# Kernel tuning notes

Hardware: AMD Instinct MI355X
Metric: run time of the kernel (lower is better)

Reference implementation:

```python
import jax, jax.numpy as jnp
import numpy as np

B, L, W = 4096, 30, 5          # batch, MAX_TOKEN_LENGTH, WINDOW_SIZE
A, E = 30, 128                 # ALPHABET_SIZE, embedding dim
C = 40                         # OUT_CHANNELS
H, T = 128, 3                  # LSTM_UNITS, num CRF tags
LIN = W * C                    # 200
EPS = 1e-5


def setup_inputs():
    key = jax.random.key(0)
    ks = jax.random.split(key, 24)
    def rn(k, shape, s=0.1):
        return jax.random.normal(k, shape, jnp.float32) * s
    return {
        'x': jax.random.randint(ks[0], (B, L, W), 0, A, jnp.int32),
        'emb': rn(ks[1], (A, E), 1.0),
        'conv_w': rn(ks[2], (C, E, 3)),
        'conv_b': rn(ks[3], (C,)),
        'bn1_g': 1.0 + rn(ks[4], (C,)),
        'bn1_b': rn(ks[5], (C,)),
        'bn1_m': rn(ks[6], (C,)),
        'bn1_v': 0.5 + jax.random.uniform(ks[7], (C,), jnp.float32),
        'w_ih_f': rn(ks[8], (4 * H, LIN)),
        'w_hh_f': rn(ks[9], (4 * H, H)),
        'b_f': rn(ks[10], (4 * H,)),
        'w_ih_b': rn(ks[11], (4 * H, LIN)),
        'w_hh_b': rn(ks[12], (4 * H, H)),
        'b_b': rn(ks[13], (4 * H,)),
        'bn2_g': 1.0 + rn(ks[14], (2 * H,)),
        'bn2_b': rn(ks[15], (2 * H,)),
        'bn2_m': rn(ks[16], (2 * H,)),
        'bn2_v': 0.5 + jax.random.uniform(ks[17], (2 * H,), jnp.float32),
        'fc_w': rn(ks[18], (T, 2 * H)),
        'fc_b': rn(ks[19], (T,)),
        'trans': rn(ks[20], (T, T)),
        'start_t': rn(ks[21], (T,)),
        'end_t': rn(ks[22], (T,)),
    }


def _lstm_dir(seq, w_ih, w_hh, b, reverse):
    # seq: [B, L, F]; torch gate order i, f, g, o
    xs = jnp.einsum('blf,gf->lbg', seq, w_ih) + b  # [L, B, 4H]
    h0 = jnp.zeros((seq.shape[0], H), seq.dtype)
    def step(carry, xt):
        h, c = carry
        z = xt + h @ w_hh.T
        i, f, g, o = jnp.split(z, 4, axis=-1)
        c = jax.nn.sigmoid(f) * c + jax.nn.sigmoid(i) * jnp.tanh(g)
        h = jax.nn.sigmoid(o) * jnp.tanh(c)
        return (h, c), h
    _, hs = jax.lax.scan(step, (h0, h0), xs, reverse=reverse)
    return hs.transpose(1, 0, 2)  # [B, L, H]


def _viterbi(emis, mask, trans, start_t, end_t):
    # emis: [B, L, T], mask: [B, L] bool
    score = start_t + emis[:, 0]                      # [B, T]
    def step(score, inp):
        e_t, m_t = inp                                # [B, T], [B]
        cand = score[:, :, None] + trans              # [B, Tprev, Tnext]
        ptr = jnp.argmax(cand, axis=1)                # [B, T]
        new = jnp.max(cand, axis=1) + e_t
        return jnp.where(m_t[:, None], new, score), ptr
    score, hist = jax.lax.scan(
        step, score, (emis[:, 1:].transpose(1, 0, 2), mask[:, 1:].T))
    score = score + end_t
    best = jnp.max(score, axis=1)                     # [B] path scores
    last = jnp.argmax(score, axis=1)                  # [B]
    def back(tag, inp):
        h_t, m_t = inp
        prev = jnp.take_along_axis(h_t, tag[:, None], axis=1)[:, 0]
        tag = jnp.where(m_t, prev, tag)
        return tag, tag
    _, ys = jax.lax.scan(back, last, (hist, mask[:, 1:].T), reverse=True)
    tags = jnp.concatenate([ys, last[None]], axis=0).T  # [B, L]
    return best, tags


def reference(x, emb, conv_w, conv_b, bn1_g, bn1_b, bn1_m, bn1_v,
              w_ih_f, w_hh_f, b_f, w_ih_b, w_hh_b, b_b,
              bn2_g, bn2_b, bn2_m, bn2_v, fc_w, fc_b, trans, start_t, end_t):
    mask = x[:, :, 2] > 0                             # [B, L]
    e = emb[x.reshape(B * L, W)]                      # [N, W, E]  (dropout=eval noop)
    e = e.transpose(0, 2, 1)                          # [N, E, W]
    y = jax.lax.conv_general_dilated(
        e, conv_w, (1,), [(1, 1)],
        dimension_numbers=('NCH', 'OIH', 'NCH')) + conv_b[:, None]
    # BatchNorm1d (inference, running stats)
    y = (y - bn1_m[:, None]) * (bn1_g / jnp.sqrt(bn1_v + EPS))[:, None] + bn1_b[:, None]
    y = jax.nn.relu(y)
    # MaxPool1d(k=3, stride=1, pad=1): length preserved
    y = jax.lax.reduce_window(y, -jnp.inf, jax.lax.max,
                              (1, 1, 3), (1, 1, 1),
                              [(0, 0), (0, 0), (1, 1)])
    y = y.reshape(B, L, LIN)                          # torch.flatten is channel-major = row-major reshape
    hf = _lstm_dir(y, w_ih_f, w_hh_f, b_f, False)
    hb = _lstm_dir(y, w_ih_b, w_hh_b, b_b, True)
    h = jnp.concatenate([hf, hb], axis=-1)            # [B, L, 2H]
    h = (h - bn2_m) * (bn2_g / jnp.sqrt(bn2_v + EPS)) + bn2_b
    emis = h @ fc_w.T + fc_b                          # [B, L, T]
    return _viterbi(emis, mask, trans, start_t, end_t)
```

## Files before the change

kernel.cpp:

```cpp
#include <hip/hip_runtime.h>
#include <math.h>

#define BB    4096
#define LL    30
#define WW    5
#define CC    40
#define HH    128
#define TT    3
#define KA    328
#define KPAD  352
#define NB    32
#define ASTR  360
#define ZSTR  520
#define CW    1056

#define WS_P    0
#define WS_BC   3600
#define WS_BG   3648
#define WS_WFC  4672
#define WS_EB   5440
#define WS_WBF  5504
#define WS_EMIS (5504 + 540672)

typedef __bf16 bf16x8 __attribute__((ext_vector_type(8)));
typedef float  f32x4  __attribute__((ext_vector_type(4)));
typedef unsigned short u16x8 __attribute__((ext_vector_type(8)));

__device__ __forceinline__ float sigm(float x) {
    return __builtin_amdgcn_rcpf(1.0f + __expf(-x));
}
__device__ __forceinline__ float tanh_fast(float x) {
    return 2.0f * __builtin_amdgcn_rcpf(1.0f + __expf(-2.0f * x)) - 1.0f;
}
__device__ __forceinline__ unsigned short f2bf(float f) {
    unsigned u = __builtin_bit_cast(unsigned, f);
    return (unsigned short)((u + 0x7FFFu + ((u >> 16) & 1u)) >> 16);
}
__device__ __forceinline__ float bf2f(unsigned short h) {
    unsigned u = ((unsigned)h) << 16;
    return __builtin_bit_cast(float, u);
}

__global__ void prep_kernel(const float* __restrict__ emb, const float* __restrict__ conv_w,
                            const float* __restrict__ conv_b,
                            const float* __restrict__ bn1_g, const float* __restrict__ bn1_b,
                            const float* __restrict__ bn1_m, const float* __restrict__ bn1_v,
                            const float* __restrict__ w_ih_f, const float* __restrict__ w_hh_f,
                            const float* __restrict__ b_f,
                            const float* __restrict__ w_ih_b, const float* __restrict__ w_hh_b,
                            const float* __restrict__ b_b,
                            const float* __restrict__ bn2_g, const float* __restrict__ bn2_b,
                            const float* __restrict__ bn2_m, const float* __restrict__ bn2_v,
                            const float* __restrict__ fc_w, const float* __restrict__ fc_b,
                            float* __restrict__ ws)
{
    const int gid = blockIdx.x * blockDim.x + threadIdx.x;
    const int gsz = gridDim.x * blockDim.x;

    for (int idx = gid; idx < 3600; idx += gsz) {
        int k = idx / 1200, rem = idx % 1200, a = rem / 40, c = rem % 40;
        float s1 = bn1_g[c] / sqrtf(bn1_v[c] + 1e-5f);
        float acc = 0.f;
        for (int e = 0; e < 128; ++e)
            acc += emb[a * 128 + e] * conv_w[(c * 128 + e) * 3 + k];
        ws[WS_P + idx] = acc * s1;
    }
    for (int c = gid; c < CC; c += gsz) {
        float s1 = bn1_g[c] / sqrtf(bn1_v[c] + 1e-5f);
        ws[WS_BC + c] = (conv_b[c] - bn1_m[c]) * s1 + bn1_b[c];
    }
    for (int i = gid; i < 1024; i += gsz) {
        int d = i >> 9, g = i & 511;
        ws[WS_BG + i] = d ? b_b[g] : b_f[g];
    }
    for (int i = gid; i < 768; i += gsz) {
        int d = i / 384, r = i % 384, t = r / 128, u = r % 128;
        int j = d * 128 + u;
        float s2 = bn2_g[j] / sqrtf(bn2_v[j] + 1e-5f);
        ws[WS_WFC + i] = fc_w[t * 256 + j] * s2;
    }
    for (int t = gid; t < TT; t += gsz) {
        float acc = fc_b[t];
        for (int j = 0; j < 256; ++j) {
            float s2 = bn2_g[j] / sqrtf(bn2_v[j] + 1e-5f);
            acc += fc_w[t * 256 + j] * (bn2_b[j] - bn2_m[j] * s2);
        }
        ws[WS_EB + t] = acc;
    }
    unsigned short* wsu = (unsigned short*)ws;
    for (int i = gid; i < 2 * 512 * CW; i += gsz) {
        int d = i / (512 * CW), r = i % (512 * CW);
        int n = r / CW, q = r % CW;
        int Ks = q / 96, t = q % 96, s = t / 32, k32 = t % 32;
        int k = Ks * 32 + k32;
        int u = n >> 2, g = n & 3, row = g * 128 + u;
        const float* wih = d ? w_ih_b : w_ih_f;
        const float* whh = d ? w_hh_b : w_hh_f;
        float w = (k < 200) ? wih[row * 200 + k]
                            : ((k < KA) ? whh[row * 128 + (k - 200)] : 0.f);
        unsigned short t0 = f2bf(w);
        float r1 = w - bf2f(t0);
        unsigned short t1 = f2bf(r1);
        unsigned short t2 = f2bf(r1 - bf2f(t1));
        wsu[2 * WS_WBF + i] = (s == 0) ? t0 : ((s == 1) ? t1 : t2);
    }
}

__global__ __launch_bounds__(512, 1)
void lstm_kernel(const int* __restrict__ x, float* __restrict__ ws)
{
    __shared__ unsigned short AhU[NB * ASTR];
    __shared__ unsigned short AlU[NB * ASTR];
    __shared__ unsigned short AmU[NB * ASTR];
    __shared__ float Zs[NB * ZSTR];
    __shared__ float Pp_s[3600];
    __shared__ float Wfc_s[384];
    __shared__ float biasC_s[40];

    const int tid = threadIdx.x;
    const int d   = blockIdx.x & 1;
    const int b0  = (blockIdx.x >> 1) * NB;

    const unsigned short* __restrict__ Wb =
        (const unsigned short*)ws + 2 * WS_WBF + d * (512 * CW);
    float* emis = ws + WS_EMIS + d * (BB * LL * TT);

    for (int i = tid; i < 3600; i += 512) Pp_s[i] = ws[WS_P + i];
    for (int i = tid; i < 384;  i += 512) Wfc_s[i] = ws[WS_WFC + d * 384 + i];
    for (int i = tid; i < 40;   i += 512) biasC_s[i] = ws[WS_BC + i];
    for (int i = tid; i < NB * ASTR / 2; i += 512) {
        ((unsigned*)AhU)[i] = 0u;
        ((unsigned*)AlU)[i] = 0u;
        ((unsigned*)AmU)[i] = 0u;
    }

    const int lane = tid & 63;
    const int wv   = tid >> 6;
    const int quad = lane >> 4;
    const int ml   = lane & 15;

    const unsigned short* __restrict__ Wn0 = Wb + (wv * 64 +  0 + ml) * CW + quad * 8;
    const unsigned short* __restrict__ Wn1 = Wb + (wv * 64 + 16 + ml) * CW + quad * 8;
    const unsigned short* __restrict__ Wn2 = Wb + (wv * 64 + 32 + ml) * CW + quad * 8;
    const unsigned short* __restrict__ Wn3 = Wb + (wv * 64 + 48 + ml) * CW + quad * 8;

    const int ug = tid & 127;
    const int rg = tid >> 7;
    const float* bgp = ws + WS_BG + d * 512;
    const float bI = bgp[ug], bF = bgp[128 + ug], bG = bgp[256 + ug], bO = bgp[384 + ug];

    float cst[8];
    #pragma unroll
    for (int i = 0; i < 8; ++i) cst[i] = 0.f;

    __syncthreads();

    for (int step = 0; step < LL; ++step) {
        const int l = d ? (LL - 1 - step) : step;

        for (int p = tid; p < NB * CC; p += 512) {
            int bb = p / CC, c = p % CC;
            const int* tok = x + (((b0 + bb) * LL) + l) * WW;
            int t0 = tok[0], t1 = tok[1], t2 = tok[2], t3 = tok[3], t4 = tok[4];
            float bc = biasC_s[c];
            float a0 = bc + Pp_s[(30 + t0) * 40 + c] + Pp_s[(60 + t1) * 40 + c];
            float a1 = bc + Pp_s[t0 * 40 + c] + Pp_s[(30 + t1) * 40 + c] + Pp_s[(60 + t2) * 40 + c];
            float a2 = bc + Pp_s[t1 * 40 + c] + Pp_s[(30 + t2) * 40 + c] + Pp_s[(60 + t3) * 40 + c];
            float a3 = bc + Pp_s[t2 * 40 + c] + Pp_s[(30 + t3) * 40 + c] + Pp_s[(60 + t4) * 40 + c];
            float a4 = bc + Pp_s[t3 * 40 + c] + Pp_s[(30 + t4) * 40 + c];
            a0 = fmaxf(a0, 0.f); a1 = fmaxf(a1, 0.f); a2 = fmaxf(a2, 0.f);
            a3 = fmaxf(a3, 0.f); a4 = fmaxf(a4, 0.f);
            float f[5];
            f[0] = fmaxf(a0, a1);
            f[1] = fmaxf(fmaxf(a0, a1), a2);
            f[2] = fmaxf(fmaxf(a1, a2), a3);
            f[3] = fmaxf(fmaxf(a2, a3), a4);
            f[4] = fmaxf(a3, a4);
            int base = bb * ASTR + c * 5;
            #pragma unroll
            for (int j = 0; j < 5; ++j) {
                unsigned short h0 = f2bf(f[j]);
                float r1 = f[j] - bf2f(h0);
                unsigned short h1 = f2bf(r1);
                unsigned short h2 = f2bf(r1 - bf2f(h1));
                AhU[base + j] = h0;
                AlU[base + j] = h1;
                AmU[base + j] = h2;
            }
        }
        __syncthreads();

        f32x4 acc[2][4];
        #pragma unroll
        for (int mt = 0; mt < 2; ++mt)
            #pragma unroll
            for (int nt = 0; nt < 4; ++nt)
                acc[mt][nt] = (f32x4){0.f, 0.f, 0.f, 0.f};

#define WLOAD(B, P, KS)                                                        \
        {                                                                      \
            B[0] = *(const bf16x8*)((P) + (KS) * 96);                          \
            B[1] = *(const bf16x8*)((P) + (KS) * 96 + 32);                     \
            B[2] = *(const bf16x8*)((P) + (KS) * 96 + 64);                     \
        }
#define GEMM6(B, NT)                                                           \
        {                                                                      \
            acc[0][NT] = __builtin_amdgcn_mfma_f32_16x16x32_bf16(a0[0], B[0], acc[0][NT], 0, 0, 0); \
            acc[0][NT] = __builtin_amdgcn_mfma_f32_16x16x32_bf16(a0[1], B[0], acc[0][NT], 0, 0, 0); \
            acc[0][NT] = __builtin_amdgcn_mfma_f32_16x16x32_bf16(a0[0], B[1], acc[0][NT], 0, 0, 0); \
            acc[0][NT] = __builtin_amdgcn_mfma_f32_16x16x32_bf16(a0[1], B[1], acc[0][NT], 0, 0, 0); \
            acc[0][NT] = __builtin_amdgcn_mfma_f32_16x16x32_bf16(a0[0], B[2], acc[0][NT], 0, 0, 0); \
            acc[0][NT] = __builtin_amdgcn_mfma_f32_16x16x32_bf16(a0[2], B[0], acc[0][NT], 0, 0, 0); \
            acc[1][NT] = __builtin_amdgcn_mfma_f32_16x16x32_bf16(a1[0], B[0], acc[1][NT], 0, 0, 0); \
            acc[1][NT] = __builtin_amdgcn_mfma_f32_16x16x32_bf16(a1[1], B[0], acc[1][NT], 0, 0, 0); \
            acc[1][NT] = __builtin_amdgcn_mfma_f32_16x16x32_bf16(a1[0], B[1], acc[1][NT], 0, 0, 0); \
            acc[1][NT] = __builtin_amdgcn_mfma_f32_16x16x32_bf16(a1[1], B[1], acc[1][NT], 0, 0, 0); \
            acc[1][NT] = __builtin_amdgcn_mfma_f32_16x16x32_bf16(a1[0], B[2], acc[1][NT], 0, 0, 0); \
            acc[1][NT] = __builtin_amdgcn_mfma_f32_16x16x32_bf16(a1[2], B[0], acc[1][NT], 0, 0, 0); \
        }

        bf16x8 bufA[3], bufB[3];
        WLOAD(bufA, Wn0, 0)

        #pragma unroll
        for (int Ks = 0; Ks < 11; ++Ks) {
            const int ko = Ks * 32 + quad * 8;
            bf16x8 a0[3], a1[3];
            a0[0] = *(const bf16x8*)&AhU[ml * ASTR + ko];
            a0[1] = *(const bf16x8*)&AlU[ml * ASTR + ko];
            a0[2] = *(const bf16x8*)&AmU[ml * ASTR + ko];
            a1[0] = *(const bf16x8*)&AhU[(16 + ml) * ASTR + ko];
            a1[1] = *(const bf16x8*)&AlU[(16 + ml) * ASTR + ko];
            a1[2] = *(const bf16x8*)&AmU[(16 + ml) * ASTR + ko];

            WLOAD(bufB, Wn1, Ks)
            GEMM6(bufA, 0)
            WLOAD(bufA, Wn2, Ks)
            GEMM6(bufB, 1)
            WLOAD(bufB, Wn3, Ks)
            GEMM6(bufA, 2)
            if (Ks < 10) WLOAD(bufA, Wn0, Ks + 1)
            GEMM6(bufB, 3)
        }
#undef WLOAD
#undef GEMM6

        #pragma unroll
        for (int mt = 0; mt < 2; ++mt)
            #pragma unroll
            for (int nt = 0; nt < 4; ++nt) {
                int col = wv * 64 + nt * 16 + ml;
                int row0 = mt * 16 + quad * 4;
                #pragma unroll
                for (int i = 0; i < 4; ++i)
                    Zs[(row0 + i) * ZSTR + col] = acc[mt][nt][i];
            }
        __syncthreads();

        #pragma unroll
        for (int i = 0; i < 8; ++i) {
            int r = rg * 8 + i;
            float4 z = *(const float4*)&Zs[r * ZSTR + ug * 4];
            float zi = z.x + bI, zf = z.y + bF, zg = z.z + bG, zo = z.w + bO;
            float cn = sigm(zf) * cst[i] + sigm(zi) * tanh_fast(zg);
            cst[i] = cn;
            float h = sigm(zo) * tanh_fast(cn);
            unsigned short h0 = f2bf(h);
            float r1 = h - bf2f(h0);
            unsigned short h1 = f2bf(r1);
            unsigned short h2 = f2bf(r1 - bf2f(h1));
            int idx = r * ASTR + 200 + ug;
            AhU[idx] = h0;
            AlU[idx] = h1;
            AmU[idx] = h2;
        }
        __syncthreads();

        if (tid < 192) {
            int bb = tid / 6, r6 = tid % 6, t = r6 >> 1, seg = r6 & 1;
            int base = bb * ASTR + 200 + seg * 64;
            const float* wfc = &Wfc_s[t * 128 + seg * 64];
            float s = 0.f;
            #pragma unroll
            for (int i = 0; i < 8; ++i) {
                u16x8 v0 = *(const u16x8*)&AhU[base + i * 8];
                u16x8 v1 = *(const u16x8*)&AlU[base + i * 8];
                u16x8 v2 = *(const u16x8*)&AmU[base + i * 8];
                #pragma unroll
                for (int j = 0; j < 8; ++j) {
                    float h = bf2f(v0[j]) + bf2f(v1[j]) + bf2f(v2[j]);
                    s += h * wfc[i * 8 + j];
                }
            }
            s += __shfl_xor(s, 1);
            if (seg == 0)
                emis[(((b0 + bb) * LL) + l) * TT + t] = s;
        }
    }
}

__global__ void viterbi_kernel(const int* __restrict__ x, const float* __restrict__ ws,
                               const float* __restrict__ trans,
                               const float* __restrict__ start_t,
                               const float* __restrict__ end_t,
                               float* __restrict__ out)
{
    int b = blockIdx.x * blockDim.x + threadIdx.x;
    if (b >= BB) return;
    const float* eF = ws + WS_EMIS;
    const float* eB = ws + WS_EMIS + BB * LL * TT;
    const float eb0 = ws[WS_EB + 0], eb1 = ws[WS_EB + 1], eb2 = ws[WS_EB + 2];
    float tr[9];
    #pragma unroll
    for (int i = 0; i < 9; ++i) tr[i] = trans[i];

    int base = b * LL * TT;
    float s0 = start_t[0] + eF[base + 0] + eB[base + 0] + eb0;
    float s1 = start_t[1] + eF[base + 1] + eB[base + 1] + eb1;
    float s2 = start_t[2] + eF[base + 2] + eB[base + 2] + eb2;

    unsigned hist[LL - 1];
    unsigned maskbits = 0;

    #pragma unroll
    for (int l = 1; l < LL; ++l) {
        bool m = x[(b * LL + l) * WW + 2] > 0;
        if (m) maskbits |= (1u << l);
        int idx = base + l * TT;
        float e0 = eF[idx + 0] + eB[idx + 0] + eb0;
        float e1 = eF[idx + 1] + eB[idx + 1] + eb1;
        float e2 = eF[idx + 2] + eB[idx + 2] + eb2;

        float ns[3]; int pt[3];
        #pragma unroll
        for (int nt = 0; nt < 3; ++nt) {
            float c0 = s0 + tr[0 * 3 + nt];
            float c1 = s1 + tr[1 * 3 + nt];
            float c2 = s2 + tr[2 * 3 + nt];
            int p = 0; float bc = c0;
            if (c1 > bc) { bc = c1; p = 1; }
            if (c2 > bc) { bc = c2; p = 2; }
            ns[nt] = bc; pt[nt] = p;
        }
        ns[0] += e0; ns[1] += e1; ns[2] += e2;
        hist[l - 1] = (unsigned)pt[0] | ((unsigned)pt[1] << 2) | ((unsigned)pt[2] << 4);
        if (m) { s0 = ns[0]; s1 = ns[1]; s2 = ns[2]; }
    }
    s0 += end_t[0]; s1 += end_t[1]; s2 += end_t[2];
    float best = s0; int last = 0;
    if (s1 > best) { best = s1; last = 1; }
    if (s2 > best) { best = s2; last = 2; }

    out[b] = best;
    float* tags = out + BB + b * LL;
    int tag = last;
    tags[LL - 1] = (float)last;
    #pragma unroll
    for (int l = LL - 1; l >= 1; --l) {
        int prev = (int)((hist[l - 1] >> (2 * tag)) & 3u);
        if (maskbits & (1u << l)) tag = prev;
        tags[l - 1] = (float)tag;
    }
}

extern "C" void kernel_launch(void* const* d_in, const int* in_sizes, int n_in,
                              void* d_out, int out_size, void* d_ws, size_t ws_size,
                              hipStream_t stream)
{
    const int*   x      = (const int*)  d_in[0];
    const float* emb    = (const float*)d_in[1];
    const float* conv_w = (const float*)d_in[2];
    const float* conv_b = (const float*)d_in[3];
    const float* bn1_g  = (const float*)d_in[4];
    const float* bn1_b  = (const float*)d_in[5];
    const float* bn1_m  = (const float*)d_in[6];
    const float* bn1_v  = (const float*)d_in[7];
    const float* w_ih_f = (const float*)d_in[8];
    const float* w_hh_f = (const float*)d_in[9];
    const float* b_f    = (const float*)d_in[10];
    const float* w_ih_b = (const float*)d_in[11];
    const float* w_hh_b = (const float*)d_in[12];
    const float* b_b    = (const float*)d_in[13];
    const float* bn2_g  = (const float*)d_in[14];
    const float* bn2_b  = (const float*)d_in[15];
    const float* bn2_m  = (const float*)d_in[16];
    const float* bn2_v  = (const float*)d_in[17];
    const float* fc_w   = (const float*)d_in[18];
    const float* fc_b   = (const float*)d_in[19];
    const float* trans  = (const float*)d_in[20];
    const float* start_t= (const float*)d_in[21];
    const float* end_t  = (const float*)d_in[22];

    float* ws  = (float*)d_ws;
    float* out = (float*)d_out;

    prep_kernel<<<256, 256, 0, stream>>>(emb, conv_w, conv_b,
                                         bn1_g, bn1_b, bn1_m, bn1_v,
                                         w_ih_f, w_hh_f, b_f,
                                         w_ih_b, w_hh_b, b_b,
                                         bn2_g, bn2_b, bn2_m, bn2_v,
                                         fc_w, fc_b, ws);
    lstm_kernel<<<256, 512, 0, stream>>>(x, ws);
    viterbi_kernel<<<16, 256, 0, stream>>>(x, ws, trans, start_t, end_t, out);
}
```

Before: 841.8 us.

## Double-buffer conv features and compute LSTM gates directly from MFMA accumulators

Splits the shared A operand into double-buffered feature tiles and a separate hidden-state tile, so the next timestep's conv features are computed while the current step's emission projection runs, before a single barrier. The MFMA operands are swapped so each lane's accumulator holds the four i,f,g,o gates of one unit, which removes the Zs shared-memory round trip and one barrier per step. The weight packing is changed so the hidden-state columns start at K offset 224. The emission output is delayed by one step and flushed after the loop, which adds some bookkeeping and extra shared memory for the second feature buffer.

```diff
diff --git a/kernel.cpp b/kernel.cpp
--- a/kernel.cpp
+++ b/kernel.cpp
@@ -8,10 +8,9 @@
 #define HH    128
 #define TT    3
 #define KA    328
-#define KPAD  352
 #define NB    32
-#define ASTR  360
-#define ZSTR  520
+#define FSTR  232
+#define HSTR  136
 #define CW    1056
 
 #define WS_P    0
@@ -97,7 +96,7 @@
         const float* wih = d ? w_ih_b : w_ih_f;
         const float* whh = d ? w_hh_b : w_hh_f;
         float w = (k < 200) ? wih[row * 200 + k]
-                            : ((k < KA) ? whh[row * 128 + (k - 200)] : 0.f);
+                            : ((k >= 224) ? whh[row * 128 + (k - 224)] : 0.f);
         unsigned short t0 = f2bf(w);
         float r1 = w - bf2f(t0);
         unsigned short t1 = f2bf(r1);
@@ -109,10 +108,8 @@
 __global__ __launch_bounds__(512, 1)
 void lstm_kernel(const int* __restrict__ x, float* __restrict__ ws)
 {
-    __shared__ unsigned short AhU[NB * ASTR];
-    __shared__ unsigned short AlU[NB * ASTR];
-    __shared__ unsigned short AmU[NB * ASTR];
-    __shared__ float Zs[NB * ZSTR];
+    __shared__ unsigned short Fh[2][NB * FSTR], Fl[2][NB * FSTR], Fm[2][NB * FSTR];
+    __shared__ unsigned short Hh[NB * HSTR], Hl[NB * HSTR], Hm[NB * HSTR];
     __shared__ float Pp_s[3600];
     __shared__ float Wfc_s[384];
     __shared__ float biasC_s[40];
@@ -128,10 +125,11 @@
     for (int i = tid; i < 3600; i += 512) Pp_s[i] = ws[WS_P + i];
     for (int i = tid; i < 384;  i += 512) Wfc_s[i] = ws[WS_WFC + d * 384 + i];
     for (int i = tid; i < 40;   i += 512) biasC_s[i] = ws[WS_BC + i];
-    for (int i = tid; i < NB * ASTR / 2; i += 512) {
-        ((unsigned*)AhU)[i] = 0u;
-        ((unsigned*)AlU)[i] = 0u;
-        ((unsigned*)AmU)[i] = 0u;
+    for (int i = tid; i < NB * FSTR; i += 512) {
+        ((unsigned*)Fh)[i] = 0u; ((unsigned*)Fl)[i] = 0u; ((unsigned*)Fm)[i] = 0u;
+    }
+    for (int i = tid; i < NB * HSTR / 2; i += 512) {
+        ((unsigned*)Hh)[i] = 0u; ((unsigned*)Hl)[i] = 0u; ((unsigned*)Hm)[i] = 0u;
     }
 
     const int lane = tid & 63;
@@ -144,51 +142,67 @@
     const unsigned short* __restrict__ Wn2 = Wb + (wv * 64 + 32 + ml) * CW + quad * 8;
     const unsigned short* __restrict__ Wn3 = Wb + (wv * 64 + 48 + ml) * CW + quad * 8;
 
-    const int ug = tid & 127;
-    const int rg = tid >> 7;
     const float* bgp = ws + WS_BG + d * 512;
-    const float bI = bgp[ug], bF = bgp[128 + ug], bG = bgp[256 + ug], bO = bgp[384 + ug];
-
-    float cst[8];
+    int   un[4];
+    float bIv[4], bFv[4], bGv[4], bOv[4];
     #pragma unroll
-    for (int i = 0; i < 8; ++i) cst[i] = 0.f;
+    for (int nt = 0; nt < 4; ++nt) {
+        int u = wv * 16 + nt * 4 + quad;
+        un[nt]  = u;
+        bIv[nt] = bgp[u];
+        bFv[nt] = bgp[128 + u];
+        bGv[nt] = bgp[256 + u];
+        bOv[nt] = bgp[384 + u];
+    }
+
+    float cst[2][4];
+    #pragma unroll
+    for (int mt = 0; mt < 2; ++mt)
+        #pragma unroll
+        for (int nt = 0; nt < 4; ++nt) cst[mt][nt] = 0.f;
 
     __syncthreads();
 
+#define DO_FEATURES(LPOS, BUF)                                                 \
+    for (int p = tid; p < NB * CC; p += 512) {                                 \
+        int bb = p / CC, c = p % CC;                                           \
+        const int* tok = x + (((b0 + bb) * LL) + (LPOS)) * WW;                 \
+        int t0 = tok[0], t1 = tok[1], t2 = tok[2], t3 = tok[3], t4 = tok[4];   \
+        float bc = biasC_s[c];                                                 \
+        float a0 = bc + Pp_s[(30 + t0) * 40 + c] + Pp_s[(60 + t1) * 40 + c];   \
+        float a1 = bc + Pp_s[t0 * 40 + c] + Pp_s[(30 + t1) * 40 + c] + Pp_s[(60 + t2) * 40 + c]; \
+        float a2 = bc + Pp_s[t1 * 40 + c] + Pp_s[(30 + t2) * 40 + c] + Pp_s[(60 + t3) * 40 + c]; \
+        float a3 = bc + Pp_s[t2 * 40 + c] + Pp_s[(30 + t3) * 40 + c] + Pp_s[(60 + t4) * 40 + c]; \
+        float a4 = bc + Pp_s[t3 * 40 + c] + Pp_s[(30 + t4) * 40 + c];          \
+        a0 = fmaxf(a0, 0.f); a1 = fmaxf(a1, 0.f); a2 = fmaxf(a2, 0.f);         \
+        a3 = fmaxf(a3, 0.f); a4 = fmaxf(a4, 0.f);                              \
+        float f[5];                                                            \
+        f[0] = fmaxf(a0, a1);                                                  \
+        f[1] = fmaxf(fmaxf(a0, a1), a2);                                       \
+        f[2] = fmaxf(fmaxf(a1, a2), a3);                                       \
+        f[3] = fmaxf(fmaxf(a2, a3), a4);                                       \
+        f[4] = fmaxf(a3, a4);                                                  \
+        int base = bb * FSTR + c * 5;                                          \
+        _Pragma("unroll")                                                      \
+        for (int j = 0; j < 5; ++j) {                                          \
+            unsigned short h0 = f2bf(f[j]);                                    \
+            float r1 = f[j] - bf2f(h0);                                        \
+            unsigned short h1 = f2bf(r1);                                      \
+            unsigned short h2 = f2bf(r1 - bf2f(h1));                           \
+            Fh[BUF][base + j] = h0;                                            \
+            Fl[BUF][base + j] = h1;                                            \
+            Fm[BUF][base + j] = h2;                                            \
+        }                                                                      \
+    }
+
+    {
+        const int l0 = d ? (LL - 1) : 0;
+        DO_FEATURES(l0, 0)
+    }
+    __syncthreads();
+
     for (int step = 0; step < LL; ++step) {
-        const int l = d ? (LL - 1 - step) : step;
-
-        for (int p = tid; p < NB * CC; p += 512) {
-            int bb = p / CC, c = p % CC;
-            const int* tok = x + (((b0 + bb) * LL) + l) * WW;
-            int t0 = tok[0], t1 = tok[1], t2 = tok[2], t3 = tok[3], t4 = tok[4];
-            float bc = biasC_s[c];
-            float a0 = bc + Pp_s[(30 + t0) * 40 + c] + Pp_s[(60 + t1) * 40 + c];
-            float a1 = bc + Pp_s[t0 * 40 + c] + Pp_s[(30 + t1) * 40 + c] + Pp_s[(60 + t2) * 40 + c];
-            float a2 = bc + Pp_s[t1 * 40 + c] + Pp_s[(30 + t2) * 40 + c] + Pp_s[(60 + t3) * 40 + c];
-            float a3 = bc + Pp_s[t2 * 40 + c] + Pp_s[(30 + t3) * 40 + c] + Pp_s[(60 + t4) * 40 + c];
-            float a4 = bc + Pp_s[t3 * 40 + c] + Pp_s[(30 + t4) * 40 + c];
-            a0 = fmaxf(a0, 0.f); a1 = fmaxf(a1, 0.f); a2 = fmaxf(a2, 0.f);
-            a3 = fmaxf(a3, 0.f); a4 = fmaxf(a4, 0.f);
-            float f[5];
-            f[0] = fmaxf(a0, a1);
-            f[1] = fmaxf(fmaxf(a0, a1), a2);
-            f[2] = fmaxf(fmaxf(a1, a2), a3);
-            f[3] = fmaxf(fmaxf(a2, a3), a4);
-            f[4] = fmaxf(a3, a4);
-            int base = bb * ASTR + c * 5;
-            #pragma unroll
-            for (int j = 0; j < 5; ++j) {
-                unsigned short h0 = f2bf(f[j]);
-                float r1 = f[j] - bf2f(h0);
-                unsigned short h1 = f2bf(r1);
-                unsigned short h2 = f2bf(r1 - bf2f(h1));
-                AhU[base + j] = h0;
-                AlU[base + j] = h1;
-                AmU[base + j] = h2;
-            }
-        }
-        __syncthreads();
+        const int fb = step & 1;
 
         f32x4 acc[2][4];
         #pragma unroll
@@ -205,87 +219,72 @@
         }
 #define GEMM6(B, NT)                                                           \
         {                                                                      \
-            acc[0][NT] = __builtin_amdgcn_mfma_f32_16x16x32_bf16(a0[0], B[0], acc[0][NT], 0, 0, 0); \
-            acc[0][NT] = __builtin_amdgcn_mfma_f32_16x16x32_bf16(a0[1], B[0], acc[0][NT], 0, 0, 0); \
-            acc[0][NT] = __builtin_amdgcn_mfma_f32_16x16x32_bf16(a0[0], B[1], acc[0][NT], 0, 0, 0); \
-            acc[0][NT] = __builtin_amdgcn_mfma_f32_16x16x32_bf16(a0[1], B[1], acc[0][NT], 0, 0, 0); \
-            acc[0][NT] = __builtin_amdgcn_mfma_f32_16x16x32_bf16(a0[0], B[2], acc[0][NT], 0, 0, 0); \
-            acc[0][NT] = __builtin_amdgcn_mfma_f32_16x16x32_bf16(a0[2], B[0], acc[0][NT], 0, 0, 0); \
-            acc[1][NT] = __builtin_amdgcn_mfma_f32_16x16x32_bf16(a1[0], B[0], acc[1][NT], 0, 0, 0); \
-            acc[1][NT] = __builtin_amdgcn_mfma_f32_16x16x32_bf16(a1[1], B[0], acc[1][NT], 0, 0, 0); \
-            acc[1][NT] = __builtin_amdgcn_mfma_f32_16x16x32_bf16(a1[0], B[1], acc[1][NT], 0, 0, 0); \
-            acc[1][NT] = __builtin_amdgcn_mfma_f32_16x16x32_bf16(a1[1], B[1], acc[1][NT], 0, 0, 0); \
-            acc[1][NT] = __builtin_amdgcn_mfma_f32_16x16x32_bf16(a1[0], B[2], acc[1][NT], 0, 0, 0); \
-            acc[1][NT] = __builtin_amdgcn_mfma_f32_16x16x32_bf16(a1[2], B[0], acc[1][NT], 0, 0, 0); \
-        }
-
-        bf16x8 bufA[3], bufB[3];
-        WLOAD(bufA, Wn0, 0)
-
-        #pragma unroll
-        for (int Ks = 0; Ks < 11; ++Ks) {
-            const int ko = Ks * 32 + quad * 8;
-            bf16x8 a0[3], a1[3];
-            a0[0] = *(const bf16x8*)&AhU[ml * ASTR + ko];
-            a0[1] = *(const bf16x8*)&AlU[ml * ASTR + ko];
-            a0[2] = *(const bf16x8*)&AmU[ml * ASTR + ko];
-            a1[0] = *(const bf16x8*)&AhU[(16 + ml) * ASTR + ko];
-            a1[1] = *(const bf16x8*)&AlU[(16 + ml) * ASTR + ko];
-            a1[2] = *(const bf16x8*)&AmU[(16 + ml) * ASTR + ko];
-
-            WLOAD(bufB, Wn1, Ks)
-            GEMM6(bufA, 0)
-            WLOAD(bufA, Wn2, Ks)
-            GEMM6(bufB, 1)
-            WLOAD(bufB, Wn3, Ks)
-            GEMM6(bufA, 2)
-            if (Ks < 10) WLOAD(bufA, Wn0, Ks + 1)
-            GEMM6(bufB, 3)
+            acc[0][NT] = __builtin_amdgcn_mfma_f32_16x16x32_bf16(B[0], a0[0], acc[0][NT], 0, 0, 0); \
+            acc[0][NT] = __builtin_amdgcn_mfma_f32_16x16x32_bf16(B[0], a0[1], acc[0][NT], 0, 0, 0); \
+            acc[0][NT] = __builtin_amdgcn_mfma_f32_16x16x32_bf16(B[1], a0[0], acc[0][NT], 0, 0, 0); \
+            acc[0][NT] = __builtin_amdgcn_mfma_f32_16x16x32_bf16(B[1], a0[1], acc[0][NT], 0, 0, 0); \
+            acc[0][NT] = __builtin_amdgcn_mfma_f32_16x16x32_bf16(B[2], a0[0], acc[0][NT], 0, 0, 0); \
+            acc[0][NT] = __builtin_amdgcn_mfma_f32_16x16x32_bf16(B[0], a0[2], acc[0][NT], 0, 0, 0); \
+            acc[1][NT] = __builtin_amdgcn_mfma_f32_16x16x32_bf16(B[0], a1[0], acc[1][NT], 0, 0, 0); \
+            acc[1][NT] = __builtin_amdgcn_mfma_f32_16x16x32_bf16(B[0], a1[1], acc[1][NT], 0, 0, 0); \
+            acc[1][NT] = __builtin_amdgcn_mfma_f32_16x16x32_bf16(B[1], a1[0], acc[1][NT], 0, 0, 0); \
+            acc[1][NT] = __builtin_amdgcn_mfma_f32_16x16x32_bf16(B[1], a1[1], acc[1][NT], 0, 0, 0); \
+            acc[1][NT] = __builtin_amdgcn_mfma_f32_16x16x32_bf16(B[2], a1[0], acc[1][NT], 0, 0, 0); \
+            acc[1][NT] = __builtin_amdgcn_mfma_f32_16x16x32_bf16(B[0], a1[2], acc[1][NT], 0, 0, 0); \
+        }
+
+        {
+            bf16x8 bufA[3], bufB[3];
+            WLOAD(bufA, Wn0, 0)
+
+            #pragma unroll
+            for (int Ks = 0; Ks < 11; ++Ks) {
+                bf16x8 a0[3], a1[3];
+                if (Ks < 7) {
+                    const int ko = Ks * 32 + quad * 8;
+                    a0[0] = *(const bf16x8*)&Fh[fb][ml * FSTR + ko];
+                    a0[1] = *(const bf16x8*)&Fl[fb][ml * FSTR + ko];
+                    a0[2] = *(const bf16x8*)&Fm[fb][ml * FSTR + ko];
+                    a1[0] = *(const bf16x8*)&Fh[fb][(16 + ml) * FSTR + ko];
+                    a1[1] = *(const bf16x8*)&Fl[fb][(16 + ml) * FSTR + ko];
+                    a1[2] = *(const bf16x8*)&Fm[fb][(16 + ml) * FSTR + ko];
+                } else {
+                    const int ko = (Ks - 7) * 32 + quad * 8;
+                    a0[0] = *(const bf16x8*)&Hh[ml * HSTR + ko];
+                    a0[1] = *(const bf16x8*)&Hl[ml * HSTR + ko];
+                    a0[2] = *(const bf16x8*)&Hm[ml * HSTR + ko];
+                    a1[0] = *(const bf16x8*)&Hh[(16 + ml) * HSTR + ko];
+                    a1[1] = *(const bf16x8*)&Hl[(16 + ml) * HSTR + ko];
+                    a1[2] = *(const bf16x8*)&Hm[(16 + ml) * HSTR + ko];
+                }
+                WLOAD(bufB, Wn1, Ks)
+                GEMM6(bufA, 0)
+                WLOAD(bufA, Wn2, Ks)
+                GEMM6(bufB, 1)
+                WLOAD(bufB, Wn3, Ks)
+                GEMM6(bufA, 2)
+                if (Ks < 10) WLOAD(bufA, Wn0, Ks + 1)
+                GEMM6(bufB, 3)
+            }
         }
 #undef WLOAD
 #undef GEMM6
 
-        #pragma unroll
-        for (int mt = 0; mt < 2; ++mt)
-            #pragma unroll
-            for (int nt = 0; nt < 4; ++nt) {
-                int col = wv * 64 + nt * 16 + ml;
-                int row0 = mt * 16 + quad * 4;
-                #pragma unroll
-                for (int i = 0; i < 4; ++i)
-                    Zs[(row0 + i) * ZSTR + col] = acc[mt][nt][i];
-            }
-        __syncthreads();
-
-        #pragma unroll
-        for (int i = 0; i < 8; ++i) {
-            int r = rg * 8 + i;
-            float4 z = *(const float4*)&Zs[r * ZSTR + ug * 4];
-            float zi = z.x + bI, zf = z.y + bF, zg = z.z + bG, zo = z.w + bO;
-            float cn = sigm(zf) * cst[i] + sigm(zi) * tanh_fast(zg);
-            cst[i] = cn;
-            float h = sigm(zo) * tanh_fast(cn);
-            unsigned short h0 = f2bf(h);
-            float r1 = h - bf2f(h0);
-            unsigned short h1 = f2bf(r1);
-            unsigned short h2 = f2bf(r1 - bf2f(h1));
-            int idx = r * ASTR + 200 + ug;
-            AhU[idx] = h0;
-            AlU[idx] = h1;
-            AmU[idx] = h2;
-        }
-        __syncthreads();
-
-        if (tid < 192) {
+        if (step + 1 < LL) {
+            const int lnext = d ? (LL - 2 - step) : (step + 1);
+            DO_FEATURES(lnext, (step + 1) & 1)
+        }
+        if (step > 0 && tid < 192) {
+            const int lprev = d ? (LL - step) : (step - 1);
             int bb = tid / 6, r6 = tid % 6, t = r6 >> 1, seg = r6 & 1;
-            int base = bb * ASTR + 200 + seg * 64;
+            int hb = bb * HSTR + seg * 64;
             const float* wfc = &Wfc_s[t * 128 + seg * 64];
             float s = 0.f;
             #pragma unroll
             for (int i = 0; i < 8; ++i) {
-                u16x8 v0 = *(const u16x8*)&AhU[base + i * 8];
-                u16x8 v1 = *(const u16x8*)&AlU[base + i * 8];
-                u16x8 v2 = *(const u16x8*)&AmU[base + i * 8];
+                u16x8 v0 = *(const u16x8*)&Hh[hb + i * 8];
+                u16x8 v1 = *(const u16x8*)&Hl[hb + i * 8];
+                u16x8 v2 = *(const u16x8*)&Hm[hb + i * 8];
                 #pragma unroll
                 for (int j = 0; j < 8; ++j) {
                     float h = bf2f(v0[j]) + bf2f(v1[j]) + bf2f(v2[j]);
@@ -294,9 +293,57 @@
             }
             s += __shfl_xor(s, 1);
             if (seg == 0)
-                emis[(((b0 + bb) * LL) + l) * TT + t] = s;
-        }
-    }
+                emis[(((b0 + bb) * LL) + lprev) * TT + t] = s;
+        }
+
+        __syncthreads();
+
+        #pragma unroll
+        for (int mt = 0; mt < 2; ++mt) {
+            #pragma unroll
+            for (int nt = 0; nt < 4; ++nt) {
+                float zi = acc[mt][nt][0] + bIv[nt];
+                float zf = acc[mt][nt][1] + bFv[nt];
+                float zg = acc[mt][nt][2] + bGv[nt];
+                float zo = acc[mt][nt][3] + bOv[nt];
+                float cn = sigm(zf) * cst[mt][nt] + sigm(zi) * tanh_fast(zg);
+                cst[mt][nt] = cn;
+                float h = sigm(zo) * tanh_fast(cn);
+                unsigned short h0 = f2bf(h);
+                float r1 = h - bf2f(h0);
+                unsigned short h1 = f2bf(r1);
+                unsigned short h2 = f2bf(r1 - bf2f(h1));
+                int idx = (mt * 16 + ml) * HSTR + un[nt];
+                Hh[idx] = h0;
+                Hl[idx] = h1;
+                Hm[idx] = h2;
+            }
+        }
+        __syncthreads();
+    }
+
+    if (tid < 192) {
+        const int llast = d ? 0 : (LL - 1);
+        int bb = tid / 6, r6 = tid % 6, t = r6 >> 1, seg = r6 & 1;
+        int hb = bb * HSTR + seg * 64;
+        const float* wfc = &Wfc_s[t * 128 + seg * 64];
+        float s = 0.f;
+        #pragma unroll
+        for (int i = 0; i < 8; ++i) {
+            u16x8 v0 = *(const u16x8*)&Hh[hb + i * 8];
+            u16x8 v1 = *(const u16x8*)&Hl[hb + i * 8];
+            u16x8 v2 = *(const u16x8*)&Hm[hb + i * 8];
+            #pragma unroll
+            for (int j = 0; j < 8; ++j) {
+                float h = bf2f(v0[j]) + bf2f(v1[j]) + bf2f(v2[j]);
+                s += h * wfc[i * 8 + j];
+            }
+        }
+        s += __shfl_xor(s, 1);
+        if (seg == 0)
+            emis[(((b0 + bb) * LL) + llast) * TT + t] = s;
+    }
+#undef DO_FEATURES
 }
 
 __global__ void viterbi_kernel(const int* __restrict__ x, const float* __restrict__ ws,
```

Result: faster. 808.6 us (-4.0%).
